# Performance work log

Hardware: AMD Instinct MI355X
Metric: run time of the kernel (lower is better)

## Reference

```python
import jax, jax.numpy as jnp
import numpy as np

B = 4096

def _conv(x, w, s):
    return jax.lax.conv_general_dilated(x, w, (s, s), 'SAME', dimension_numbers=('NHWC', 'HWIO', 'NHWC'))

def _convT(x, w, s):
    return jax.lax.conv_transpose(x, w, (s, s), 'SAME', dimension_numbers=('NHWC', 'HWIO', 'NHWC'))

def _otsu(error):
    # faithful to the TF source: 81 candidate thresholds in [0.1, 0.9],
    # counts of NONZERO masked entries (not simple class counts), NaN-guarded means,
    thresholds = jnp.asarray(np.arange(0.1, 0.91, 0.01), dtype=jnp.float32)  # 81
    hw = error.shape[1] * error.shape[2]
    zero = jnp.zeros(error.shape[0], jnp.float32)

    def step(carry, t):
        sig_max, opti = carry
        below = error < t
        e0 = jnp.where(below, error, 0.0)
        e1 = jnp.where(below, 0.0, error)
        n0 = jnp.sum((e0 != 0).astype(jnp.float32), axis=(1, 2))
        n1 = jnp.sum((e1 != 0).astype(jnp.float32), axis=(1, 2))
        m0 = (jnp.sum(e0, axis=(1, 2)) / hw) * ((n1 + n0) / n0)
        m0 = jnp.where(jnp.isnan(m0), 0.0, m0)
        m1 = (jnp.sum(e1, axis=(1, 2)) / hw) * ((n1 + n0) / n1)
        m1 = jnp.where(jnp.isnan(m1), 0.0, m1)
        p0 = n0 / (n0 + n1)
        p1 = n1 / (n0 + n1)
        sig_b = p0 * p1 * (m0 - m1) ** 2
        upd = sig_b >= sig_max
        return (jnp.where(upd, sig_b, sig_max), jnp.where(upd, t, opti)), None

    (_, opti), _ = jax.lax.scan(step, (zero, zero), thresholds)
    return opti

def _forward(x, eps_noise, ew1, eb1, es1, eo1, ew2, eb2, es2, eo2, ew3, eb3, es3, eo3,
             wzm, bzm, wzl, bzl, dw, db, tw1, tb1, ds1, do1, tw2, tb2, ds2, do2,
             tw3, tb3, ds3, do3, tw4, tb4):
    relu = jax.nn.relu
    # encoder; inference-mode BatchNorm folded into per-channel scale/offset
    h = relu(_conv(x, ew1, 2) + eb1) * es1 + eo1            # [B,16,16,32]
    h = relu(_conv(h, ew2, 2) + eb2) * es2 + eo2            # [B,8,8,64]
    h = relu(_conv(h, ew3, 2) + eb3) * es3 + eo3            # [B,4,4,128]
    h = h.reshape(h.shape[0], -1)                           # [B,2048]
    z_mean = relu(h @ wzm + bzm)
    z_log_var = relu(h @ wzl + bzl)
    z = z_mean + jnp.exp(0.5 * z_log_var) * eps_noise       # Sampling layer
    # decoder (Dropout is identity at inference)
    d = relu(z @ dw + db).reshape(-1, 8, 8, 128)
    d = relu(_convT(d, tw1, 1) + tb1) * ds1 + do1           # [B,8,8,128]
    d = relu(_convT(d, tw2, 2) + tb2) * ds2 + do2           # [B,16,16,64]
    d = relu(_convT(d, tw3, 2) + tb3) * ds3 + do3           # [B,32,32,32]
    recon = jax.nn.sigmoid(_convT(d, tw4, 1) + tb4)         # [B,32,32,3]
    error = jnp.mean((x - recon) ** 2, axis=-1)             # [B,32,32]
    thresh = _otsu(error)                                   # [B]
    return error < thresh[:, None, None]                    # bool mask

def setup_inputs():
    key = jax.random.key(0)
    ks = jax.random.split(key, 12)
    f = jnp.float32
    s = 0.05  # small init scale to keep activations sane
    d = {}
    d['x'] = jax.random.uniform(ks[0], (B, 32, 32, 3), f)
    d['eps_noise'] = jax.random.normal(ks[1], (B, 128), f)
    d['ew1'] = jax.random.normal(ks[2], (5, 5, 3, 32), f) * s
    d['eb1'] = jnp.zeros((32,), f); d['es1'] = jnp.ones((32,), f); d['eo1'] = jnp.zeros((32,), f)
    d['ew2'] = jax.random.normal(ks[3], (5, 5, 32, 64), f) * s
    d['eb2'] = jnp.zeros((64,), f); d['es2'] = jnp.ones((64,), f); d['eo2'] = jnp.zeros((64,), f)
    d['ew3'] = jax.random.normal(ks[4], (5, 5, 64, 128), f) * s
    d['eb3'] = jnp.zeros((128,), f); d['es3'] = jnp.ones((128,), f); d['eo3'] = jnp.zeros((128,), f)
    d['wzm'] = jax.random.normal(ks[5], (2048, 128), f) * s
    d['bzm'] = jnp.zeros((128,), f)
    d['wzl'] = jax.random.normal(ks[6], (2048, 128), f) * s
    d['bzl'] = jnp.zeros((128,), f)
    d['dw'] = jax.random.normal(ks[7], (128, 8192), f) * s
    d['db'] = jnp.zeros((8192,), f)
    d['tw1'] = jax.random.normal(ks[8], (1, 1, 128, 128), f) * s
    d['tb1'] = jnp.zeros((128,), f); d['ds1'] = jnp.ones((128,), f); d['do1'] = jnp.zeros((128,), f)
    d['tw2'] = jax.random.normal(ks[9], (3, 3, 128, 64), f) * s
    d['tb2'] = jnp.zeros((64,), f); d['ds2'] = jnp.ones((64,), f); d['do2'] = jnp.zeros((64,), f)
    d['tw3'] = jax.random.normal(ks[10], (3, 3, 64, 32), f) * s
    d['tb3'] = jnp.zeros((32,), f); d['ds3'] = jnp.ones((32,), f); d['do3'] = jnp.zeros((32,), f)
    d['tw4'] = jax.random.normal(ks[11], (3, 3, 32, 3), f) * s
    d['tb4'] = jnp.zeros((3,), f)
    return d

def reference(x, eps_noise, ew1, eb1, es1, eo1, ew2, eb2, es2, eo2, ew3, eb3, es3, eo3,
              wzm, bzm, wzl, bzl, dw, db, tw1, tb1, ds1, do1, tw2, tb2, ds2, do2,
              tw3, tb3, ds3, do3, tw4, tb4):
    mask = _forward(x, eps_noise, ew1, eb1, es1, eo1, ew2, eb2, es2, eo2, ew3, eb3, es3, eo3,
                    wzm, bzm, wzl, bzl, dw, db, tw1, tb1, ds1, do1, tw2, tb2, ds2, do2,
                    tw3, tb3, ds3, do3, tw4, tb4)
    return mask.astype(jnp.int32)
```

## Files before the change

### kernel.cpp

```cpp
#include <hip/hip_runtime.h>
#include <cstdint>
#include <cstddef>


__global__ __launch_bounds__(256) void k_conv1(const float* __restrict__ x,
    const float* __restrict__ w, const float* __restrict__ bb,
    const float* __restrict__ sc, const float* __restrict__ of,
    float* __restrict__ out) {
  const int b = blockIdx.x;
  const int pos = threadIdx.x;
  const int oy = pos >> 4, ox = pos & 15;
  float acc[32];
#pragma unroll
  for (int c = 0; c < 32; ++c) acc[c] = 0.f;
  const float* xb = x + (size_t)b * 3072;
#pragma unroll 1
  for (int ky = 0; ky < 5; ++ky) {
    const int iy = 2 * oy - 1 + ky;
    if ((unsigned)iy >= 32u) continue;
#pragma unroll 1
    for (int kx = 0; kx < 5; ++kx) {
      const int ix = 2 * ox - 1 + kx;
      if ((unsigned)ix >= 32u) continue;
      const float* xp = xb + (iy * 32 + ix) * 3;
#pragma unroll
      for (int ci = 0; ci < 3; ++ci) {
        const float v = xp[ci];
        const float* wp = w + ((ky * 5 + kx) * 3 + ci) * 32;
#pragma unroll
        for (int c = 0; c < 32; ++c) acc[c] = fmaf(v, wp[c], acc[c]);
      }
    }
  }
  float* op = out + ((size_t)b * 256 + pos) * 32;
#pragma unroll
  for (int c = 0; c < 32; ++c) {
    const float v = fmaxf(acc[c] + bb[c], 0.f);
    op[c] = v * sc[c] + of[c];
  }
}

__global__ __launch_bounds__(256) void k_conv2(const float* __restrict__ in,
    const float* __restrict__ w, const float* __restrict__ bb,
    const float* __restrict__ sc, const float* __restrict__ of,
    float* __restrict__ out) {
  __shared__ float tile[8192];
  const int b = blockIdx.x;
  const int tid = threadIdx.x;
#pragma unroll
  for (int q = 0; q < 8; ++q) {
    const int f4 = tid + q * 256;
    const int pix = f4 >> 3, c4 = (f4 & 7) << 2;
    const float4 v = ((const float4*)(in + (size_t)b * 8192))[f4];
    const int s = ((pix >> 4) * 5 + (pix & 15)) & 31;
    float* dst = &tile[pix * 32];
    dst[(c4 + 0) ^ s] = v.x; dst[(c4 + 1) ^ s] = v.y;
    dst[(c4 + 2) ^ s] = v.z; dst[(c4 + 3) ^ s] = v.w;
  }
  __syncthreads();
  const int pos = tid & 63;
  const int ch = __builtin_amdgcn_readfirstlane(tid >> 6) * 16;
  const int oy = pos >> 3, ox = pos & 7;
  float acc[16];
#pragma unroll
  for (int c = 0; c < 16; ++c) acc[c] = 0.f;
#pragma unroll 1
  for (int ky = 0; ky < 5; ++ky) {
    const int iy = 2 * oy - 1 + ky;
#pragma unroll 1
    for (int kx = 0; kx < 5; ++kx) {
      const int ix = 2 * ox - 1 + kx;
      const bool valid = ((unsigned)iy < 16u) && ((unsigned)ix < 16u);
      const int pix = valid ? (iy * 16 + ix) : 0;
      const int s = ((pix >> 4) * 5 + (pix & 15)) & 31;
      const float* tp = &tile[pix * 32];
      const float* wrow = w + ((ky * 5 + kx) * 32) * 64 + ch;
#pragma unroll 4
      for (int ci = 0; ci < 32; ++ci) {
        float v = tp[ci ^ s];
        v = valid ? v : 0.f;
        const float* wp = wrow + ci * 64;
#pragma unroll
        for (int c = 0; c < 16; ++c) acc[c] = fmaf(v, wp[c], acc[c]);
      }
    }
  }
  float* op = out + ((size_t)b * 64 + pos) * 64 + ch;
#pragma unroll
  for (int c = 0; c < 16; ++c) {
    const float v = fmaxf(acc[c] + bb[ch + c], 0.f);
    op[c] = v * sc[ch + c] + of[ch + c];
  }
}

__global__ __launch_bounds__(512) void k_conv3(const float* __restrict__ in,
    const float* __restrict__ w, const float* __restrict__ bb,
    const float* __restrict__ sc, const float* __restrict__ of,
    float* __restrict__ out) {
  __shared__ float tile[4 * 4096];
  const int b0 = blockIdx.x * 4;
  const int tid = threadIdx.x;
#pragma unroll
  for (int q = 0; q < 8; ++q) {
    const int f4 = tid + q * 512;
    const int img = f4 >> 10, rem = f4 & 1023;
    const int pix = rem >> 4, c4 = (rem & 15) << 2;
    const float4 v = ((const float4*)(in + (size_t)(b0 + img) * 4096))[rem];
    const int s = ((pix >> 3) * 5 + (pix & 7) + img * 9) & 31;
    float* dst = &tile[img * 4096 + pix * 64];
    dst[(c4 + 0) ^ s] = v.x; dst[(c4 + 1) ^ s] = v.y;
    dst[(c4 + 2) ^ s] = v.z; dst[(c4 + 3) ^ s] = v.w;
  }
  __syncthreads();
  const int lane = tid & 63;
  const int pos = lane & 15, img = lane >> 4;
  const int ch = __builtin_amdgcn_readfirstlane(tid >> 6) * 16;
  const int oy = pos >> 2, ox = pos & 3;
  float acc[16];
#pragma unroll
  for (int c = 0; c < 16; ++c) acc[c] = 0.f;
  const float* tb = &tile[img * 4096];
#pragma unroll 1
  for (int ky = 0; ky < 5; ++ky) {
    const int iy = 2 * oy - 1 + ky;
#pragma unroll 1
    for (int kx = 0; kx < 5; ++kx) {
      const int ix = 2 * ox - 1 + kx;
      const bool valid = ((unsigned)iy < 8u) && ((unsigned)ix < 8u);
      const int pix = valid ? (iy * 8 + ix) : 0;
      const int s = ((pix >> 3) * 5 + (pix & 7) + img * 9) & 31;
      const float* tp = tb + pix * 64;
      const float* wrow = w + ((ky * 5 + kx) * 64) * 128 + ch;
#pragma unroll 4
      for (int ci = 0; ci < 64; ++ci) {
        float v = tp[ci ^ s];
        v = valid ? v : 0.f;
        const float* wp = wrow + ci * 128;
#pragma unroll
        for (int c = 0; c < 16; ++c) acc[c] = fmaf(v, wp[c], acc[c]);
      }
    }
  }
  float* op = out + ((size_t)(b0 + img) * 16 + pos) * 128 + ch;
#pragma unroll
  for (int c = 0; c < 16; ++c) {
    const float v = fmaxf(acc[c] + bb[ch + c], 0.f);
    op[c] = v * sc[ch + c] + of[ch + c];
  }
}

__global__ __launch_bounds__(256) void k_fcz(const float* __restrict__ h3,
    const float* __restrict__ wzm, const float* __restrict__ bzm,
    const float* __restrict__ wzl, const float* __restrict__ bzl,
    const float* __restrict__ eps, float* __restrict__ z) {
  __shared__ float a[4 * 256];
  const int ib = blockIdx.x * 4;
  const int tid = threadIdx.x;
  const int co = tid & 127;
  const int grp = __builtin_amdgcn_readfirstlane(tid >> 7);
  float am[2], al[2];
#pragma unroll
  for (int i = 0; i < 2; ++i) { am[i] = 0.f; al[i] = 0.f; }
  for (int kc = 0; kc < 2048; kc += 256) {
    __syncthreads();
    {
      const int r = tid >> 6, c4 = (tid & 63) << 2;
      *(float4*)&a[r * 256 + c4] =
          *(const float4*)&h3[(size_t)(ib + r) * 2048 + kc + c4];
    }
    __syncthreads();
#pragma unroll 4
    for (int k = 0; k < 256; k += 4) {
      float wm[4], wl[4];
#pragma unroll
      for (int q = 0; q < 4; ++q) {
        wm[q] = wzm[(size_t)(kc + k + q) * 128 + co];
        wl[q] = wzl[(size_t)(kc + k + q) * 128 + co];
      }
#pragma unroll
      for (int i = 0; i < 2; ++i) {
        const float4 av = *(const float4*)&a[(grp * 2 + i) * 256 + k];
        am[i] = fmaf(av.x, wm[0], am[i]); am[i] = fmaf(av.y, wm[1], am[i]);
        am[i] = fmaf(av.z, wm[2], am[i]); am[i] = fmaf(av.w, wm[3], am[i]);
        al[i] = fmaf(av.x, wl[0], al[i]); al[i] = fmaf(av.y, wl[1], al[i]);
        al[i] = fmaf(av.z, wl[2], al[i]); al[i] = fmaf(av.w, wl[3], al[i]);
      }
    }
  }
#pragma unroll
  for (int i = 0; i < 2; ++i) {
    const int row = ib + grp * 2 + i;
    const float zm = fmaxf(am[i] + bzm[co], 0.f);
    const float zl = fmaxf(al[i] + bzl[co], 0.f);
    z[(size_t)row * 128 + co] = zm + expf(0.5f * zl) * eps[(size_t)row * 128 + co];
  }
}

__global__ __launch_bounds__(256) void k_fcdec(const float* __restrict__ z,
    const float* __restrict__ dw, const float* __restrict__ db,
    float* __restrict__ out) {
  __shared__ float zt[64 * 128];
  const int bid = blockIdx.x;
  const int m0 = (bid >> 6) * 64;
  const int n0 = (bid & 63) * 128;
  const int tid = threadIdx.x;
#pragma unroll
  for (int q = 0; q < 8; ++q) {
    const int f4 = tid + q * 256;
    const int img = f4 >> 5, c4 = (f4 & 31) << 2;
    const float4 v = *(const float4*)&z[(size_t)(m0 + img) * 128 + c4];
    const int s = img & 31;
    float* dst = &zt[img * 128];
    dst[(c4 + 0) ^ s] = v.x; dst[(c4 + 1) ^ s] = v.y;
    dst[(c4 + 2) ^ s] = v.z; dst[(c4 + 3) ^ s] = v.w;
  }
  __syncthreads();
  const int img = tid & 63;
  const int grp = __builtin_amdgcn_readfirstlane(tid >> 6);
  const int nb = n0 + grp * 32;
  float acc[32];
#pragma unroll
  for (int c = 0; c < 32; ++c) acc[c] = 0.f;
  const float* zrow = &zt[img * 128];
  const int s = img & 31;
#pragma unroll 4
  for (int k = 0; k < 128; ++k) {
    const float v = zrow[k ^ s];
    const float* wp = dw + (size_t)k * 8192 + nb;
#pragma unroll
    for (int c = 0; c < 32; ++c) acc[c] = fmaf(v, wp[c], acc[c]);
  }
  float* op = out + (size_t)(m0 + img) * 8192 + nb;
#pragma unroll
  for (int c = 0; c < 32; ++c) op[c] = fmaxf(acc[c] + db[nb + c], 0.f);
}

__global__ __launch_bounds__(256) void k_tconv1(const float* __restrict__ in,
    const float* __restrict__ w, const float* __restrict__ bb,
    const float* __restrict__ sc, const float* __restrict__ of,
    float* __restrict__ out) {
  __shared__ float tile[8192];
  const int b = blockIdx.x;
  const int tid = threadIdx.x;
#pragma unroll
  for (int q = 0; q < 8; ++q) {
    const int f4 = tid + q * 256;
    const int pix = f4 >> 5, c4 = (f4 & 31) << 2;
    const float4 v = ((const float4*)(in + (size_t)b * 8192))[f4];
    const int s = pix & 31;
    float* dst = &tile[pix * 128];
    dst[(c4 + 0) ^ s] = v.x; dst[(c4 + 1) ^ s] = v.y;
    dst[(c4 + 2) ^ s] = v.z; dst[(c4 + 3) ^ s] = v.w;
  }
  __syncthreads();
  const int pos = tid & 63;
  const int ch = __builtin_amdgcn_readfirstlane((tid >> 6) * 32);
  const float* trow = &tile[pos * 128];
  const int s = pos & 31;
  float acc[32];
#pragma unroll
  for (int c = 0; c < 32; ++c) acc[c] = 0.f;
#pragma unroll 4
  for (int ci = 0; ci < 128; ++ci) {
    const float v = trow[ci ^ s];
    const float* wp = w + ci * 128 + ch;
#pragma unroll
    for (int c = 0; c < 32; ++c) acc[c] = fmaf(v, wp[c], acc[c]);
  }
  float* op = out + ((size_t)b * 64 + pos) * 128 + ch;
#pragma unroll
  for (int c = 0; c < 32; ++c) {
    const float v = fmaxf(acc[c] + bb[ch + c], 0.f);
    op[c] = v * sc[ch + c] + of[ch + c];
  }
}

__global__ __launch_bounds__(256) void k_tconv2(const float* __restrict__ in,
    const float* __restrict__ w, const float* __restrict__ bb,
    const float* __restrict__ sc, const float* __restrict__ of,
    float* __restrict__ out) {
  __shared__ float tile[64 * 128];
  const int b = blockIdx.x;
  const int tid = threadIdx.x;
#pragma unroll
  for (int q = 0; q < 8; ++q) {
    const int f4 = tid + q * 256;
    const int pix = f4 >> 5, c4 = (f4 & 31) << 2;
    const float4 v = ((const float4*)(in + (size_t)b * 8192))[f4];
    const int s = ((pix >> 3) * 5 + (pix & 7)) & 31;
    float* dst = &tile[pix * 128];
    dst[(c4 + 0) ^ s] = v.x; dst[(c4 + 1) ^ s] = v.y;
    dst[(c4 + 2) ^ s] = v.z; dst[(c4 + 3) ^ s] = v.w;
  }
  __syncthreads();
  const int lane = tid & 63;
  const int ch = __builtin_amdgcn_readfirstlane((tid >> 6) * 16);
  const int jy = lane >> 3, jx = lane & 7;
  float acc[4][16];
#pragma unroll
  for (int p = 0; p < 4; ++p)
#pragma unroll
    for (int c = 0; c < 16; ++c) acc[p][c] = 0.f;
  const int DY[9]  = {1,1,0,0,1,0,0,0,0};
  const int DX[9]  = {1,0,1,0,0,0,1,0,0};
  const int KYt[9] = {0,0,2,2,0,2,1,1,1};
  const int KXt[9] = {0,2,0,2,1,1,0,2,1};
  const int PHt[9] = {0,0,0,0,1,1,2,2,3};
#pragma unroll
  for (int t = 0; t < 9; ++t) {
    const int sy = jy - DY[t], sx = jx - DX[t];
    const bool valid = (sy >= 0) && (sx >= 0);
    const int pix = valid ? (sy * 8 + sx) : 0;
    const int s = ((pix >> 3) * 5 + (pix & 7)) & 31;
    const float* tp = &tile[pix * 128];
    const float* wrow = w + ((KYt[t] * 3 + KXt[t]) * 128) * 64 + ch;
#pragma unroll 4
    for (int ci = 0; ci < 128; ++ci) {
      float v = tp[ci ^ s];
      v = valid ? v : 0.f;
      const float* wp = wrow + ci * 64;
#pragma unroll
      for (int c = 0; c < 16; ++c)
        acc[PHt[t]][c] = fmaf(v, wp[c], acc[PHt[t]][c]);
    }
  }
#pragma unroll
  for (int py = 0; py < 2; ++py)
#pragma unroll
    for (int px = 0; px < 2; ++px) {
      const int oy = 2 * jy + py, ox = 2 * jx + px;
      float* op = out + (((size_t)b * 16 + oy) * 16 + ox) * 64 + ch;
#pragma unroll
      for (int c = 0; c < 16; ++c) {
        const float v = fmaxf(acc[py * 2 + px][c] + bb[ch + c], 0.f);
        op[c] = v * sc[ch + c] + of[ch + c];
      }
    }
}

__global__ __launch_bounds__(256) void k_tconv3(const float* __restrict__ in,
    const float* __restrict__ w, const float* __restrict__ bb,
    const float* __restrict__ sc, const float* __restrict__ of,
    float* __restrict__ out) {
  __shared__ float tile[9 * 16 * 64];
  const int b = blockIdx.x >> 1;
  const int r0 = (blockIdx.x & 1) * 8;
  const int tid = threadIdx.x;
#pragma unroll
  for (int q = 0; q < 9; ++q) {
    const int f4 = tid + q * 256;
    const int rr = f4 >> 8, rem = f4 & 255;
    const int col = rem >> 4, c4 = (rem & 15) << 2;
    const int gy = r0 - 1 + rr;
    float4 v = make_float4(0.f, 0.f, 0.f, 0.f);
    if (gy >= 0)
      v = *(const float4*)&in[(((size_t)b * 16 + gy) * 16 + col) * 64 + c4];
    const int s = (rr * 5 + col) & 31;
    float* dst = &tile[(rr * 16 + col) * 64];
    dst[(c4 + 0) ^ s] = v.x; dst[(c4 + 1) ^ s] = v.y;
    dst[(c4 + 2) ^ s] = v.z; dst[(c4 + 3) ^ s] = v.w;
  }
  __syncthreads();
  const int pos = tid & 127;
  const int jy = pos >> 4, jx = pos & 15;
  const int ch = __builtin_amdgcn_readfirstlane(tid >> 7) * 16;
  float acc[4][16];
#pragma unroll
  for (int p = 0; p < 4; ++p)
#pragma unroll
    for (int c = 0; c < 16; ++c) acc[p][c] = 0.f;
  const int DY[9]  = {1,1,0,0,1,0,0,0,0};
  const int DX[9]  = {1,0,1,0,0,0,1,0,0};
  const int KYt[9] = {0,0,2,2,0,2,1,1,1};
  const int KXt[9] = {0,2,0,2,1,1,0,2,1};
  const int PHt[9] = {0,0,0,0,1,1,2,2,3};
#pragma unroll
  for (int t = 0; t < 9; ++t) {
    const int syst = jy + 1 - DY[t];
    const int sx = jx - DX[t];
    const bool valid = (sx >= 0);
    const int sxc = valid ? sx : 0;
    const int s = (syst * 5 + sxc) & 31;
    const float* tp = &tile[(syst * 16 + sxc) * 64];
    const float* wrow = w + ((KYt[t] * 3 + KXt[t]) * 64) * 32 + ch;
#pragma unroll 2
    for (int ci = 0; ci < 64; ++ci) {
      float v = tp[ci ^ s];
      v = valid ? v : 0.f;
      const float* wp = wrow + ci * 32;
#pragma unroll
      for (int c = 0; c < 16; ++c)
        acc[PHt[t]][c] = fmaf(v, wp[c], acc[PHt[t]][c]);
    }
  }
  const int gy = r0 + jy;
#pragma unroll
  for (int py = 0; py < 2; ++py)
#pragma unroll
    for (int px = 0; px < 2; ++px) {
      const int oy = 2 * gy + py, ox = 2 * jx + px;
      float* op = out + (((size_t)b * 32 + oy) * 32 + ox) * 32 + ch;
#pragma unroll
      for (int c = 0; c < 16; ++c) {
        const float v = fmaxf(acc[py * 2 + px][c] + bb[ch + c], 0.f);
        op[c] = v * sc[ch + c] + of[ch + c];
      }
    }
}

__global__ __launch_bounds__(128) void k_tconv4err(const float* __restrict__ t3,
    const float* __restrict__ w, const float* __restrict__ bb,
    const float* __restrict__ x, float* __restrict__ err) {
  __shared__ float tile[32 * 340];
  const int b = blockIdx.x >> 2;
  const int r0 = (blockIdx.x & 3) * 8;
  const int tid = threadIdx.x;
  for (int f4 = tid; f4 < 2560; f4 += 128) {
    const int rr = f4 >> 8, rem = f4 & 255;
    const int px = rem >> 3, c4 = (rem & 7) << 2;
    const int gy = r0 - 1 + rr;
    float4 v = make_float4(0.f, 0.f, 0.f, 0.f);
    if ((unsigned)gy < 32u)
      v = *(const float4*)&t3[(((size_t)b * 32 + gy) * 32 + px) * 32 + c4];
    tile[(c4 + 0) * 340 + rr * 34 + px] = v.x;
    tile[(c4 + 1) * 340 + rr * 34 + px] = v.y;
    tile[(c4 + 2) * 340 + rr * 34 + px] = v.z;
    tile[(c4 + 3) * 340 + rr * 34 + px] = v.w;
  }
  __syncthreads();
  const int tx = tid & 31, ty = tid >> 5;
  float acc[2][3];
#pragma unroll
  for (int d = 0; d < 2; ++d)
#pragma unroll
    for (int c = 0; c < 3; ++c) acc[d][c] = 0.f;
#pragma unroll 2
  for (int ci = 0; ci < 32; ++ci) {
    float p[4][3];
#pragma unroll
    for (int r = 0; r < 4; ++r)
#pragma unroll
      for (int cx = 0; cx < 3; ++cx) {
        const int lx = tx + cx - 1;
        float v = 0.f;
        if ((unsigned)lx < 32u) v = tile[ci * 340 + (ty * 2 + r) * 34 + lx];
        p[r][cx] = v;
      }
#pragma unroll
    for (int ky = 0; ky < 3; ++ky)
#pragma unroll
      for (int kx = 0; kx < 3; ++kx) {
        const float* wp = w + ((ky * 3 + kx) * 32 + ci) * 3;
#pragma unroll
        for (int dy = 0; dy < 2; ++dy) {
          const float v = p[dy + ky][kx];
          acc[dy][0] = fmaf(v, wp[0], acc[dy][0]);
          acc[dy][1] = fmaf(v, wp[1], acc[dy][1]);
          acc[dy][2] = fmaf(v, wp[2], acc[dy][2]);
        }
      }
  }
#pragma unroll
  for (int dy = 0; dy < 2; ++dy) {
    const int oy = r0 + ty * 2 + dy;
    const size_t pidx = (size_t)b * 1024 + oy * 32 + tx;
    float e = 0.f;
#pragma unroll
    for (int c = 0; c < 3; ++c) {
      const float pre = acc[dy][c] + bb[c];
      float r;
      if (pre >= 0.f) {
        r = 1.f / (1.f + expf(-pre));
      } else {
        const float ex = expf(pre);
        r = ex / (1.f + ex);
      }
      const float dd = x[pidx * 3 + c] - r;
      e += dd * dd;
    }
    err[pidx] = e / 3.0f;
  }
}

__global__ __launch_bounds__(256) void k_otsu(const float* __restrict__ err,
                                              int* __restrict__ outmask) {
  __shared__ float e[2][1024];
  __shared__ float sig[2][81];
  __shared__ float opti[2];
  const int b0 = blockIdx.x * 2;
  const int tid = threadIdx.x;
  for (int f4 = tid; f4 < 512; f4 += 256) {
    const int img = f4 >> 8, idx = (f4 & 255) << 2;
    *(float4*)&e[img][idx] = *(const float4*)&err[(size_t)(b0 + img) * 1024 + idx];
  }
  __syncthreads();
  const int img = tid >> 7, j = tid & 127;
  if (j < 81) {
    const float t = (float)(0.1 + (double)j * 0.01);
    float n0 = 0.f, n1 = 0.f, s0 = 0.f, s1 = 0.f;
    for (int i = 0; i < 1024; ++i) {
      const float v = e[img][i];
      if (v < t) {
        if (v != 0.f) { n0 += 1.f; s0 += v; }
      } else {
        n1 += 1.f; s1 += v;
      }
    }
    const float nt = n0 + n1;
    float m0 = (s0 / 1024.f) * (nt / n0);
    if (m0 != m0) m0 = 0.f;
    float m1 = (s1 / 1024.f) * (nt / n1);
    if (m1 != m1) m1 = 0.f;
    const float p0 = n0 / nt, p1 = n1 / nt;
    const float dm = m0 - m1;
    sig[img][j] = p0 * p1 * (dm * dm);
  }
  __syncthreads();
  if (j == 0) {
    float smax = 0.f, op = 0.f;
    for (int jj = 0; jj < 81; ++jj) {
      const float sb = sig[img][jj];
      const float t = (float)(0.1 + (double)jj * 0.01);
      if (sb >= smax) { smax = sb; op = t; }
    }
    opti[img] = op;
  }
  __syncthreads();
#pragma unroll
  for (int q = 0; q < 8; ++q) {
    const int idx = tid + q * 256;
    const int im = idx >> 10, p = idx & 1023;
    outmask[(size_t)(b0 + im) * 1024 + p] = (e[im][p] < opti[im]) ? 1 : 0;
  }
}

extern "C" void kernel_launch(void* const* d_in, const int* in_sizes, int n_in,
                              void* d_out, int out_size, void* d_ws, size_t ws_size,
                              hipStream_t stream) {
  (void)in_sizes; (void)n_in; (void)out_size;
  const float* x    = (const float*)d_in[0];
  const float* eps  = (const float*)d_in[1];
  const float* ew1  = (const float*)d_in[2];
  const float* eb1  = (const float*)d_in[3];
  const float* es1  = (const float*)d_in[4];
  const float* eo1  = (const float*)d_in[5];
  const float* ew2  = (const float*)d_in[6];
  const float* eb2  = (const float*)d_in[7];
  const float* es2  = (const float*)d_in[8];
  const float* eo2  = (const float*)d_in[9];
  const float* ew3  = (const float*)d_in[10];
  const float* eb3  = (const float*)d_in[11];
  const float* es3  = (const float*)d_in[12];
  const float* eo3  = (const float*)d_in[13];
  const float* wzm  = (const float*)d_in[14];
  const float* bzm  = (const float*)d_in[15];
  const float* wzl  = (const float*)d_in[16];
  const float* bzl  = (const float*)d_in[17];
  const float* dw   = (const float*)d_in[18];
  const float* db   = (const float*)d_in[19];
  const float* tw1  = (const float*)d_in[20];
  const float* tb1  = (const float*)d_in[21];
  const float* ds1  = (const float*)d_in[22];
  const float* do1  = (const float*)d_in[23];
  const float* tw2  = (const float*)d_in[24];
  const float* tb2  = (const float*)d_in[25];
  const float* ds2  = (const float*)d_in[26];
  const float* do2  = (const float*)d_in[27];
  const float* tw3  = (const float*)d_in[28];
  const float* tb3  = (const float*)d_in[29];
  const float* ds3  = (const float*)d_in[30];
  const float* do3  = (const float*)d_in[31];
  const float* tw4  = (const float*)d_in[32];
  const float* tb4  = (const float*)d_in[33];
  int* mask = (int*)d_out;

  const size_t per_img_bytes = 233472;
  int C = 64;
  const int cand[6] = {4096, 2048, 1024, 512, 256, 128};
  for (int i = 0; i < 6; ++i) {
    if ((size_t)cand[i] * per_img_bytes <= ws_size) { C = cand[i]; break; }
  }

  float* p0 = (float*)d_ws;
  float* p1 = p0 + (size_t)C * 32768;
  float* p2 = p1 + (size_t)C * 8192;
  float* p3 = p2 + (size_t)C * 16384;

  for (int c0 = 0; c0 < 4096; c0 += C) {
    const float* xc   = x   + (size_t)c0 * 3072;
    const float* epsc = eps + (size_t)c0 * 128;
    int*         mc   = mask + (size_t)c0 * 1024;
    float* h1 = p0;  float* dd = p0;  float* t3 = p0;
    float* h2 = p1;  float* zz = p1;  float* t1 = p1;
    float* h3 = p2;  float* t2 = p2;
    float* er = p3;

    k_conv1    <<<C,      256, 0, stream>>>(xc, ew1, eb1, es1, eo1, h1);
    k_conv2    <<<C,      256, 0, stream>>>(h1, ew2, eb2, es2, eo2, h2);
    k_conv3    <<<C / 4,  512, 0, stream>>>(h2, ew3, eb3, es3, eo3, h3);
    k_fcz      <<<C / 4,  256, 0, stream>>>(h3, wzm, bzm, wzl, bzl, epsc, zz);
    k_fcdec    <<<C,      256, 0, stream>>>(zz, dw, db, dd);
    k_tconv1   <<<C,      256, 0, stream>>>(dd, tw1, tb1, ds1, do1, t1);
    k_tconv2   <<<C,      256, 0, stream>>>(t1, tw2, tb2, ds2, do2, t2);
    k_tconv3   <<<C * 2,  256, 0, stream>>>(t2, tw3, tb3, ds3, do3, t3);
    k_tconv4err<<<C * 4,  128, 0, stream>>>(t3, tw4, tb4, xc, er);
    k_otsu     <<<C / 2,  256, 0, stream>>>(er, mc);
  }
}
```

Measured before the change: 4.349 ms.

## Vectorize LDS reads as float4 and restructure decoder tail convolutions

Result: slower. 5.088 ms (+17.0%).

```diff
diff --git a/kernel.cpp b/kernel.cpp
--- a/kernel.cpp
+++ b/kernel.cpp
@@ -44,22 +44,20 @@
     const float* __restrict__ w, const float* __restrict__ bb,
     const float* __restrict__ sc, const float* __restrict__ of,
     float* __restrict__ out) {
-  __shared__ float tile[8192];
+  __shared__ float4 tile4[2048];
   const int b = blockIdx.x;
   const int tid = threadIdx.x;
 #pragma unroll
   for (int q = 0; q < 8; ++q) {
     const int f4 = tid + q * 256;
-    const int pix = f4 >> 3, c4 = (f4 & 7) << 2;
-    const float4 v = ((const float4*)(in + (size_t)b * 8192))[f4];
-    const int s = ((pix >> 4) * 5 + (pix & 15)) & 31;
-    float* dst = &tile[pix * 32];
-    dst[(c4 + 0) ^ s] = v.x; dst[(c4 + 1) ^ s] = v.y;
-    dst[(c4 + 2) ^ s] = v.z; dst[(c4 + 3) ^ s] = v.w;
+    const int pix = f4 >> 3, g4 = f4 & 7;
+    const int s4 = (((pix >> 4) * 5) + (pix & 15)) & 7;
+    tile4[pix * 8 + (g4 ^ s4)] = ((const float4*)(in + (size_t)b * 8192))[f4];
   }
   __syncthreads();
   const int pos = tid & 63;
-  const int ch = __builtin_amdgcn_readfirstlane(tid >> 6) * 16;
+  const int chg = __builtin_amdgcn_readfirstlane(tid >> 6);
+  const int co0 = chg * 16;
   const int oy = pos >> 3, ox = pos & 7;
   float acc[16];
 #pragma unroll
@@ -72,24 +70,28 @@
       const int ix = 2 * ox - 1 + kx;
       const bool valid = ((unsigned)iy < 16u) && ((unsigned)ix < 16u);
       const int pix = valid ? (iy * 16 + ix) : 0;
-      const int s = ((pix >> 4) * 5 + (pix & 15)) & 31;
-      const float* tp = &tile[pix * 32];
-      const float* wrow = w + ((ky * 5 + kx) * 32) * 64 + ch;
-#pragma unroll 4
-      for (int ci = 0; ci < 32; ++ci) {
-        float v = tp[ci ^ s];
-        v = valid ? v : 0.f;
-        const float* wp = wrow + ci * 64;
-#pragma unroll
-        for (int c = 0; c < 16; ++c) acc[c] = fmaf(v, wp[c], acc[c]);
-      }
-    }
-  }
-  float* op = out + ((size_t)b * 64 + pos) * 64 + ch;
+      const int s4 = (((pix >> 4) * 5) + (pix & 15)) & 7;
+      const float* wt = w + ((size_t)(ky * 5 + kx) * 32) * 64 + co0;
+#pragma unroll
+      for (int g4 = 0; g4 < 8; ++g4) {
+        float4 a = tile4[pix * 8 + (g4 ^ s4)];
+        a.x = valid ? a.x : 0.f; a.y = valid ? a.y : 0.f;
+        a.z = valid ? a.z : 0.f; a.w = valid ? a.w : 0.f;
+        const float av[4] = {a.x, a.y, a.z, a.w};
+#pragma unroll
+        for (int j = 0; j < 4; ++j) {
+          const float* wp = wt + (g4 * 4 + j) * 64;
+#pragma unroll
+          for (int c = 0; c < 16; ++c) acc[c] = fmaf(av[j], wp[c], acc[c]);
+        }
+      }
+    }
+  }
+  float* op = out + ((size_t)b * 64 + pos) * 64 + co0;
 #pragma unroll
   for (int c = 0; c < 16; ++c) {
-    const float v = fmaxf(acc[c] + bb[ch + c], 0.f);
-    op[c] = v * sc[ch + c] + of[ch + c];
+    const float v = fmaxf(acc[c] + bb[co0 + c], 0.f);
+    op[c] = v * sc[co0 + c] + of[co0 + c];
   }
 }
 
@@ -97,29 +99,28 @@
     const float* __restrict__ w, const float* __restrict__ bb,
     const float* __restrict__ sc, const float* __restrict__ of,
     float* __restrict__ out) {
-  __shared__ float tile[4 * 4096];
+  __shared__ float4 tile4[4096];
   const int b0 = blockIdx.x * 4;
   const int tid = threadIdx.x;
 #pragma unroll
   for (int q = 0; q < 8; ++q) {
     const int f4 = tid + q * 512;
     const int img = f4 >> 10, rem = f4 & 1023;
-    const int pix = rem >> 4, c4 = (rem & 15) << 2;
-    const float4 v = ((const float4*)(in + (size_t)(b0 + img) * 4096))[rem];
-    const int s = ((pix >> 3) * 5 + (pix & 7) + img * 9) & 31;
-    float* dst = &tile[img * 4096 + pix * 64];
-    dst[(c4 + 0) ^ s] = v.x; dst[(c4 + 1) ^ s] = v.y;
-    dst[(c4 + 2) ^ s] = v.z; dst[(c4 + 3) ^ s] = v.w;
+    const int pix = rem >> 4, g4 = rem & 15;
+    const int s4 = (((pix >> 3) * 5) + (pix & 7) + img * 3) & 15;
+    tile4[img * 1024 + pix * 16 + (g4 ^ s4)] =
+        ((const float4*)(in + (size_t)(b0 + img) * 4096))[rem];
   }
   __syncthreads();
   const int lane = tid & 63;
-  const int pos = lane & 15, img = lane >> 4;
-  const int ch = __builtin_amdgcn_readfirstlane(tid >> 6) * 16;
+  const int img = lane >> 4, pos = lane & 15;
+  const int chg = __builtin_amdgcn_readfirstlane(tid >> 6);
+  const int co0 = chg * 16;
   const int oy = pos >> 2, ox = pos & 3;
   float acc[16];
 #pragma unroll
   for (int c = 0; c < 16; ++c) acc[c] = 0.f;
-  const float* tb = &tile[img * 4096];
+  const float4* tb = &tile4[img * 1024];
 #pragma unroll 1
   for (int ky = 0; ky < 5; ++ky) {
     const int iy = 2 * oy - 1 + ky;
@@ -128,24 +129,28 @@
       const int ix = 2 * ox - 1 + kx;
       const bool valid = ((unsigned)iy < 8u) && ((unsigned)ix < 8u);
       const int pix = valid ? (iy * 8 + ix) : 0;
-      const int s = ((pix >> 3) * 5 + (pix & 7) + img * 9) & 31;
-      const float* tp = tb + pix * 64;
-      const float* wrow = w + ((ky * 5 + kx) * 64) * 128 + ch;
-#pragma unroll 4
-      for (int ci = 0; ci < 64; ++ci) {
-        float v = tp[ci ^ s];
-        v = valid ? v : 0.f;
-        const float* wp = wrow + ci * 128;
-#pragma unroll
-        for (int c = 0; c < 16; ++c) acc[c] = fmaf(v, wp[c], acc[c]);
-      }
-    }
-  }
-  float* op = out + ((size_t)(b0 + img) * 16 + pos) * 128 + ch;
+      const int s4 = (((pix >> 3) * 5) + (pix & 7) + img * 3) & 15;
+      const float* wt = w + ((size_t)(ky * 5 + kx) * 64) * 128 + co0;
+#pragma unroll
+      for (int g4 = 0; g4 < 16; ++g4) {
+        float4 a = tb[pix * 16 + (g4 ^ s4)];
+        a.x = valid ? a.x : 0.f; a.y = valid ? a.y : 0.f;
+        a.z = valid ? a.z : 0.f; a.w = valid ? a.w : 0.f;
+        const float av[4] = {a.x, a.y, a.z, a.w};
+#pragma unroll
+        for (int j = 0; j < 4; ++j) {
+          const float* wp = wt + (g4 * 4 + j) * 128;
+#pragma unroll
+          for (int c = 0; c < 16; ++c) acc[c] = fmaf(av[j], wp[c], acc[c]);
+        }
+      }
+    }
+  }
+  float* op = out + ((size_t)(b0 + img) * 16 + pos) * 128 + co0;
 #pragma unroll
   for (int c = 0; c < 16; ++c) {
-    const float v = fmaxf(acc[c] + bb[ch + c], 0.f);
-    op[c] = v * sc[ch + c] + of[ch + c];
+    const float v = fmaxf(acc[c] + bb[co0 + c], 0.f);
+    op[c] = v * sc[co0 + c] + of[co0 + c];
   }
 }
 
@@ -199,7 +204,7 @@
 __global__ __launch_bounds__(256) void k_fcdec(const float* __restrict__ z,
     const float* __restrict__ dw, const float* __restrict__ db,
     float* __restrict__ out) {
-  __shared__ float zt[64 * 128];
+  __shared__ float4 zt4[2048];
   const int bid = blockIdx.x;
   const int m0 = (bid >> 6) * 64;
   const int n0 = (bid & 63) * 128;
@@ -207,28 +212,28 @@
 #pragma unroll
   for (int q = 0; q < 8; ++q) {
     const int f4 = tid + q * 256;
-    const int img = f4 >> 5, c4 = (f4 & 31) << 2;
-    const float4 v = *(const float4*)&z[(size_t)(m0 + img) * 128 + c4];
-    const int s = img & 31;
-    float* dst = &zt[img * 128];
-    dst[(c4 + 0) ^ s] = v.x; dst[(c4 + 1) ^ s] = v.y;
-    dst[(c4 + 2) ^ s] = v.z; dst[(c4 + 3) ^ s] = v.w;
+    const int img = f4 >> 5, g4 = f4 & 31;
+    const int s4 = (img * 5) & 31;
+    zt4[img * 32 + (g4 ^ s4)] = ((const float4*)(z + (size_t)(m0) * 128))[f4];
   }
   __syncthreads();
   const int img = tid & 63;
   const int grp = __builtin_amdgcn_readfirstlane(tid >> 6);
   const int nb = n0 + grp * 32;
+  const int s4 = (img * 5) & 31;
   float acc[32];
 #pragma unroll
   for (int c = 0; c < 32; ++c) acc[c] = 0.f;
-  const float* zrow = &zt[img * 128];
-  const int s = img & 31;
-#pragma unroll 4
-  for (int k = 0; k < 128; ++k) {
-    const float v = zrow[k ^ s];
-    const float* wp = dw + (size_t)k * 8192 + nb;
-#pragma unroll
-    for (int c = 0; c < 32; ++c) acc[c] = fmaf(v, wp[c], acc[c]);
+#pragma unroll
+  for (int g4 = 0; g4 < 32; ++g4) {
+    const float4 a = zt4[img * 32 + (g4 ^ s4)];
+    const float av[4] = {a.x, a.y, a.z, a.w};
+#pragma unroll
+    for (int j = 0; j < 4; ++j) {
+      const float* wp = dw + (size_t)(g4 * 4 + j) * 8192 + nb;
+#pragma unroll
+      for (int c = 0; c < 32; ++c) acc[c] = fmaf(av[j], wp[c], acc[c]);
+    }
   }
   float* op = out + (size_t)(m0 + img) * 8192 + nb;
 #pragma unroll
@@ -239,39 +244,40 @@
     const float* __restrict__ w, const float* __restrict__ bb,
     const float* __restrict__ sc, const float* __restrict__ of,
     float* __restrict__ out) {
-  __shared__ float tile[8192];
+  __shared__ float4 tile4[2048];
   const int b = blockIdx.x;
   const int tid = threadIdx.x;
 #pragma unroll
   for (int q = 0; q < 8; ++q) {
     const int f4 = tid + q * 256;
-    const int pix = f4 >> 5, c4 = (f4 & 31) << 2;
-    const float4 v = ((const float4*)(in + (size_t)b * 8192))[f4];
-    const int s = pix & 31;
-    float* dst = &tile[pix * 128];
-    dst[(c4 + 0) ^ s] = v.x; dst[(c4 + 1) ^ s] = v.y;
-    dst[(c4 + 2) ^ s] = v.z; dst[(c4 + 3) ^ s] = v.w;
+    const int pix = f4 >> 5, g4 = f4 & 31;
+    const int s4 = (pix * 5) & 31;
+    tile4[pix * 32 + (g4 ^ s4)] = ((const float4*)(in + (size_t)b * 8192))[f4];
   }
   __syncthreads();
   const int pos = tid & 63;
-  const int ch = __builtin_amdgcn_readfirstlane((tid >> 6) * 32);
-  const float* trow = &tile[pos * 128];
-  const int s = pos & 31;
+  const int chg = __builtin_amdgcn_readfirstlane(tid >> 6);
+  const int co0 = chg * 32;
+  const int s4 = (pos * 5) & 31;
   float acc[32];
 #pragma unroll
   for (int c = 0; c < 32; ++c) acc[c] = 0.f;
-#pragma unroll 4
-  for (int ci = 0; ci < 128; ++ci) {
-    const float v = trow[ci ^ s];
-    const float* wp = w + ci * 128 + ch;
-#pragma unroll
-    for (int c = 0; c < 32; ++c) acc[c] = fmaf(v, wp[c], acc[c]);
-  }
-  float* op = out + ((size_t)b * 64 + pos) * 128 + ch;
+#pragma unroll
+  for (int g4 = 0; g4 < 32; ++g4) {
+    const float4 a = tile4[pos * 32 + (g4 ^ s4)];
+    const float av[4] = {a.x, a.y, a.z, a.w};
+#pragma unroll
+    for (int j = 0; j < 4; ++j) {
+      const float* wp = w + (g4 * 4 + j) * 128 + co0;
+#pragma unroll
+      for (int c = 0; c < 32; ++c) acc[c] = fmaf(av[j], wp[c], acc[c]);
+    }
+  }
+  float* op = out + ((size_t)b * 64 + pos) * 128 + co0;
 #pragma unroll
   for (int c = 0; c < 32; ++c) {
-    const float v = fmaxf(acc[c] + bb[ch + c], 0.f);
-    op[c] = v * sc[ch + c] + of[ch + c];
+    const float v = fmaxf(acc[c] + bb[co0 + c], 0.f);
+    op[c] = v * sc[co0 + c] + of[co0 + c];
   }
 }
 
@@ -279,23 +285,21 @@
     const float* __restrict__ w, const float* __restrict__ bb,
     const float* __restrict__ sc, const float* __restrict__ of,
     float* __restrict__ out) {
-  __shared__ float tile[64 * 128];
+  __shared__ float4 tile4[2048];
   const int b = blockIdx.x;
   const int tid = threadIdx.x;
 #pragma unroll
   for (int q = 0; q < 8; ++q) {
     const int f4 = tid + q * 256;
-    const int pix = f4 >> 5, c4 = (f4 & 31) << 2;
-    const float4 v = ((const float4*)(in + (size_t)b * 8192))[f4];
-    const int s = ((pix >> 3) * 5 + (pix & 7)) & 31;
-    float* dst = &tile[pix * 128];
-    dst[(c4 + 0) ^ s] = v.x; dst[(c4 + 1) ^ s] = v.y;
-    dst[(c4 + 2) ^ s] = v.z; dst[(c4 + 3) ^ s] = v.w;
-  }
-  __syncthreads();
-  const int lane = tid & 63;
-  const int ch = __builtin_amdgcn_readfirstlane((tid >> 6) * 16);
-  const int jy = lane >> 3, jx = lane & 7;
+    const int pix = f4 >> 5, g4 = f4 & 31;
+    const int s4 = (pix * 5) & 31;
+    tile4[pix * 32 + (g4 ^ s4)] = ((const float4*)(in + (size_t)b * 8192))[f4];
+  }
+  __syncthreads();
+  const int pos = tid & 63;
+  const int chg = __builtin_amdgcn_readfirstlane(tid >> 6);
+  const int co0 = chg * 16;
+  const int jy = pos >> 3, jx = pos & 7;
   float acc[4][16];
 #pragma unroll
   for (int p = 0; p < 4; ++p)
@@ -306,22 +310,26 @@
   const int KYt[9] = {0,0,2,2,0,2,1,1,1};
   const int KXt[9] = {0,2,0,2,1,1,0,2,1};
   const int PHt[9] = {0,0,0,0,1,1,2,2,3};
-#pragma unroll
+#pragma unroll 1
   for (int t = 0; t < 9; ++t) {
     const int sy = jy - DY[t], sx = jx - DX[t];
     const bool valid = (sy >= 0) && (sx >= 0);
     const int pix = valid ? (sy * 8 + sx) : 0;
-    const int s = ((pix >> 3) * 5 + (pix & 7)) & 31;
-    const float* tp = &tile[pix * 128];
-    const float* wrow = w + ((KYt[t] * 3 + KXt[t]) * 128) * 64 + ch;
-#pragma unroll 4
-    for (int ci = 0; ci < 128; ++ci) {
-      float v = tp[ci ^ s];
-      v = valid ? v : 0.f;
-      const float* wp = wrow + ci * 64;
-#pragma unroll
-      for (int c = 0; c < 16; ++c)
-        acc[PHt[t]][c] = fmaf(v, wp[c], acc[PHt[t]][c]);
+    const int s4 = (pix * 5) & 31;
+    const int ph = PHt[t];
+    const float* wt = w + ((size_t)(KYt[t] * 3 + KXt[t]) * 128) * 64 + co0;
+#pragma unroll
+    for (int g4 = 0; g4 < 32; ++g4) {
+      float4 a = tile4[pix * 32 + (g4 ^ s4)];
+      a.x = valid ? a.x : 0.f; a.y = valid ? a.y : 0.f;
+      a.z = valid ? a.z : 0.f; a.w = valid ? a.w : 0.f;
+      const float av[4] = {a.x, a.y, a.z, a.w};
+#pragma unroll
+      for (int j = 0; j < 4; ++j) {
+        const float* wp = wt + (g4 * 4 + j) * 64;
+#pragma unroll
+        for (int c = 0; c < 16; ++c) acc[ph][c] = fmaf(av[j], wp[c], acc[ph][c]);
+      }
     }
   }
 #pragma unroll
@@ -329,157 +337,179 @@
 #pragma unroll
     for (int px = 0; px < 2; ++px) {
       const int oy = 2 * jy + py, ox = 2 * jx + px;
-      float* op = out + (((size_t)b * 16 + oy) * 16 + ox) * 64 + ch;
+      float* op = out + (((size_t)b * 16 + oy) * 16 + ox) * 64 + co0;
 #pragma unroll
       for (int c = 0; c < 16; ++c) {
-        const float v = fmaxf(acc[py * 2 + px][c] + bb[ch + c], 0.f);
-        op[c] = v * sc[ch + c] + of[ch + c];
-      }
-    }
-}
-
-__global__ __launch_bounds__(256) void k_tconv3(const float* __restrict__ in,
+        const float v = fmaxf(acc[py * 2 + px][c] + bb[co0 + c], 0.f);
+        op[c] = v * sc[co0 + c] + of[co0 + c];
+      }
+    }
+}
+
+__global__ __launch_bounds__(512) void k_tconv3(const float* __restrict__ in,
     const float* __restrict__ w, const float* __restrict__ bb,
     const float* __restrict__ sc, const float* __restrict__ of,
-    float* __restrict__ out) {
-  __shared__ float tile[9 * 16 * 64];
+    float* __restrict__ t3g) {
+  __shared__ float4 tile4[145 * 16];
   const int b = blockIdx.x >> 1;
   const int r0 = (blockIdx.x & 1) * 8;
   const int tid = threadIdx.x;
-#pragma unroll
-  for (int q = 0; q < 9; ++q) {
-    const int f4 = tid + q * 256;
-    const int rr = f4 >> 8, rem = f4 & 255;
-    const int col = rem >> 4, c4 = (rem & 15) << 2;
+  for (int f4 = tid; f4 < 2304; f4 += 512) {
+    const int rr = f4 >> 8;
+    const int col = (f4 >> 4) & 15, g4 = f4 & 15;
     const int gy = r0 - 1 + rr;
     float4 v = make_float4(0.f, 0.f, 0.f, 0.f);
     if (gy >= 0)
-      v = *(const float4*)&in[(((size_t)b * 16 + gy) * 16 + col) * 64 + c4];
-    const int s = (rr * 5 + col) & 31;
-    float* dst = &tile[(rr * 16 + col) * 64];
-    dst[(c4 + 0) ^ s] = v.x; dst[(c4 + 1) ^ s] = v.y;
-    dst[(c4 + 2) ^ s] = v.z; dst[(c4 + 3) ^ s] = v.w;
-  }
+      v = *(const float4*)&in[(((size_t)b * 16 + gy) * 16 + col) * 64 + g4 * 4];
+    const int s4 = (rr * 5 + col) & 15;
+    tile4[(rr * 16 + col) * 16 + (g4 ^ s4)] = v;
+  }
+  if (tid < 16) tile4[144 * 16 + tid] = make_float4(0.f, 0.f, 0.f, 0.f);
   __syncthreads();
   const int pos = tid & 127;
-  const int jy = pos >> 4, jx = pos & 15;
-  const int ch = __builtin_amdgcn_readfirstlane(tid >> 7) * 16;
-  float acc[4][16];
+  const int prow = pos >> 4, pcol = pos & 15;
+  const int chg = __builtin_amdgcn_readfirstlane(tid >> 7);
+  const int co0 = chg * 8;
+  float acc[4][8];
 #pragma unroll
   for (int p = 0; p < 4; ++p)
 #pragma unroll
-    for (int c = 0; c < 16; ++c) acc[p][c] = 0.f;
+    for (int c = 0; c < 8; ++c) acc[p][c] = 0.f;
   const int DY[9]  = {1,1,0,0,1,0,0,0,0};
   const int DX[9]  = {1,0,1,0,0,0,1,0,0};
   const int KYt[9] = {0,0,2,2,0,2,1,1,1};
   const int KXt[9] = {0,2,0,2,1,1,0,2,1};
   const int PHt[9] = {0,0,0,0,1,1,2,2,3};
-#pragma unroll
+#pragma unroll 1
   for (int t = 0; t < 9; ++t) {
-    const int syst = jy + 1 - DY[t];
-    const int sx = jx - DX[t];
-    const bool valid = (sx >= 0);
-    const int sxc = valid ? sx : 0;
-    const int s = (syst * 5 + sxc) & 31;
-    const float* tp = &tile[(syst * 16 + sxc) * 64];
-    const float* wrow = w + ((KYt[t] * 3 + KXt[t]) * 64) * 32 + ch;
-#pragma unroll 2
-    for (int ci = 0; ci < 64; ++ci) {
-      float v = tp[ci ^ s];
-      v = valid ? v : 0.f;
-      const float* wp = wrow + ci * 32;
-#pragma unroll
-      for (int c = 0; c < 16; ++c)
-        acc[PHt[t]][c] = fmaf(v, wp[c], acc[PHt[t]][c]);
-    }
-  }
-  const int gy = r0 + jy;
+    const int syst = prow + 1 - DY[t];
+    const int sx = pcol - DX[t];
+    const bool vx = (sx >= 0);
+    const int pix = vx ? (syst * 16 + sx) : 144;
+    const int s4 = vx ? ((syst * 5 + sx) & 15) : 0;
+    const int ph = PHt[t];
+    const float* wt = w + ((size_t)(KYt[t] * 3 + KXt[t]) * 64) * 32 + co0;
+#pragma unroll
+    for (int g4 = 0; g4 < 16; ++g4) {
+      const float4 a = tile4[pix * 16 + (g4 ^ s4)];
+      const float av[4] = {a.x, a.y, a.z, a.w};
+#pragma unroll
+      for (int j = 0; j < 4; ++j) {
+        const float* wp = wt + (g4 * 4 + j) * 32;
+#pragma unroll
+        for (int c = 0; c < 8; ++c) acc[ph][c] = fmaf(av[j], wp[c], acc[ph][c]);
+      }
+    }
+  }
+  const int jy = r0 + prow;
 #pragma unroll
   for (int py = 0; py < 2; ++py)
 #pragma unroll
     for (int px = 0; px < 2; ++px) {
-      const int oy = 2 * gy + py, ox = 2 * jx + px;
-      float* op = out + (((size_t)b * 32 + oy) * 32 + ox) * 32 + ch;
-#pragma unroll
-      for (int c = 0; c < 16; ++c) {
-        const float v = fmaxf(acc[py * 2 + px][c] + bb[ch + c], 0.f);
-        op[c] = v * sc[ch + c] + of[ch + c];
-      }
-    }
-}
-
-__global__ __launch_bounds__(128) void k_tconv4err(const float* __restrict__ t3,
+      const int oy = 2 * jy + py, ox = 2 * pcol + px;
+      float* op = t3g + ((size_t)b * 4 + chg) * 8192 + (size_t)(oy * 32 + ox) * 8;
+      float vv[8];
+#pragma unroll
+      for (int c = 0; c < 8; ++c) {
+        const float v = fmaxf(acc[py * 2 + px][c] + bb[co0 + c], 0.f);
+        vv[c] = v * sc[co0 + c] + of[co0 + c];
+      }
+      *(float4*)&op[0] = make_float4(vv[0], vv[1], vv[2], vv[3]);
+      *(float4*)&op[4] = make_float4(vv[4], vv[5], vv[6], vv[7]);
+    }
+}
+
+__global__ __launch_bounds__(256) void k_tconv4err(const float* __restrict__ t3g,
     const float* __restrict__ w, const float* __restrict__ bb,
     const float* __restrict__ x, float* __restrict__ err) {
-  __shared__ float tile[32 * 340];
-  const int b = blockIdx.x >> 2;
-  const int r0 = (blockIdx.x & 3) * 8;
-  const int tid = threadIdx.x;
-  for (int f4 = tid; f4 < 2560; f4 += 128) {
-    const int rr = f4 >> 8, rem = f4 & 255;
-    const int px = rem >> 3, c4 = (rem & 7) << 2;
-    const int gy = r0 - 1 + rr;
-    float4 v = make_float4(0.f, 0.f, 0.f, 0.f);
-    if ((unsigned)gy < 32u)
-      v = *(const float4*)&t3[(((size_t)b * 32 + gy) * 32 + px) * 32 + c4];
-    tile[(c4 + 0) * 340 + rr * 34 + px] = v.x;
-    tile[(c4 + 1) * 340 + rr * 34 + px] = v.y;
-    tile[(c4 + 2) * 340 + rr * 34 + px] = v.z;
-    tile[(c4 + 3) * 340 + rr * 34 + px] = v.w;
-  }
-  __syncthreads();
-  const int tx = tid & 31, ty = tid >> 5;
-  float acc[2][3];
-#pragma unroll
-  for (int d = 0; d < 2; ++d)
-#pragma unroll
-    for (int c = 0; c < 3; ++c) acc[d][c] = 0.f;
-#pragma unroll 2
-  for (int ci = 0; ci < 32; ++ci) {
-    float p[4][3];
-#pragma unroll
-    for (int r = 0; r < 4; ++r)
-#pragma unroll
-      for (int cx = 0; cx < 3; ++cx) {
-        const int lx = tx + cx - 1;
-        float v = 0.f;
-        if ((unsigned)lx < 32u) v = tile[ci * 340 + (ty * 2 + r) * 34 + lx];
-        p[r][cx] = v;
-      }
-#pragma unroll
-    for (int ky = 0; ky < 3; ++ky)
-#pragma unroll
-      for (int kx = 0; kx < 3; ++kx) {
-        const float* wp = w + ((ky * 3 + kx) * 32 + ci) * 3;
-#pragma unroll
-        for (int dy = 0; dy < 2; ++dy) {
-          const float v = p[dy + ky][kx];
-          acc[dy][0] = fmaf(v, wp[0], acc[dy][0]);
-          acc[dy][1] = fmaf(v, wp[1], acc[dy][1]);
-          acc[dy][2] = fmaf(v, wp[2], acc[dy][2]);
+  __shared__ float4 win4[34 * 65];
+  const int b = blockIdx.x;
+  const int tid = threadIdx.x;
+  const int ty = tid >> 4, tx = tid & 15;
+  float acc[2][2][3];
+#pragma unroll
+  for (int dy = 0; dy < 2; ++dy)
+#pragma unroll
+    for (int dx = 0; dx < 2; ++dx)
+#pragma unroll
+      for (int c = 0; c < 3; ++c) acc[dy][dx][c] = 0.f;
+#pragma unroll 1
+  for (int g = 0; g < 4; ++g) {
+    __syncthreads();
+    for (int f4 = tid; f4 < 2176; f4 += 256) {
+      const int rr = f4 >> 6;
+      const int rem = f4 & 63;
+      const int col = rem >> 1, h = rem & 1;
+      const int gy = rr - 1;
+      float4 v = make_float4(0.f, 0.f, 0.f, 0.f);
+      if ((unsigned)gy < 32u)
+        v = ((const float4*)(t3g + ((size_t)b * 4 + g) * 8192))[(gy * 32 + col) * 2 + h];
+      win4[rr * 65 + col * 2 + h] = v;
+    }
+    __syncthreads();
+#pragma unroll 1
+    for (int h = 0; h < 2; ++h) {
+      float4 W[4][4];
+#pragma unroll
+      for (int wy = 0; wy < 4; ++wy)
+#pragma unroll
+        for (int wx = 0; wx < 4; ++wx) {
+          const int col = 2 * tx - 1 + wx;
+          const bool edge = (wx == 0) || (wx == 3);
+          const bool v = edge ? ((unsigned)col < 32u) : true;
+          const int cc = v ? col : 0;
+          float4 t = win4[(2 * ty + wy) * 65 + cc * 2 + h];
+          if (edge) {
+            t.x = v ? t.x : 0.f; t.y = v ? t.y : 0.f;
+            t.z = v ? t.z : 0.f; t.w = v ? t.w : 0.f;
+          }
+          W[wy][wx] = t;
         }
-      }
-  }
-#pragma unroll
-  for (int dy = 0; dy < 2; ++dy) {
-    const int oy = r0 + ty * 2 + dy;
-    const size_t pidx = (size_t)b * 1024 + oy * 32 + tx;
-    float e = 0.f;
-#pragma unroll
-    for (int c = 0; c < 3; ++c) {
-      const float pre = acc[dy][c] + bb[c];
-      float r;
-      if (pre >= 0.f) {
-        r = 1.f / (1.f + expf(-pre));
-      } else {
-        const float ex = expf(pre);
-        r = ex / (1.f + ex);
-      }
-      const float dd = x[pidx * 3 + c] - r;
-      e += dd * dd;
-    }
-    err[pidx] = e / 3.0f;
-  }
+#pragma unroll
+      for (int j = 0; j < 4; ++j) {
+        const int ci = g * 8 + h * 4 + j;
+#pragma unroll
+        for (int ky = 0; ky < 3; ++ky)
+#pragma unroll
+          for (int kx = 0; kx < 3; ++kx) {
+            const float* wp = w + ((ky * 3 + kx) * 32 + ci) * 3;
+            const float w0 = wp[0], w1 = wp[1], w2 = wp[2];
+#pragma unroll
+            for (int dy = 0; dy < 2; ++dy)
+#pragma unroll
+              for (int dx = 0; dx < 2; ++dx) {
+                const float4 t = W[dy + ky][dx + kx];
+                const float av = (j == 0) ? t.x : (j == 1) ? t.y : (j == 2) ? t.z : t.w;
+                acc[dy][dx][0] = fmaf(av, w0, acc[dy][dx][0]);
+                acc[dy][dx][1] = fmaf(av, w1, acc[dy][dx][1]);
+                acc[dy][dx][2] = fmaf(av, w2, acc[dy][dx][2]);
+              }
+          }
+      }
+    }
+  }
+#pragma unroll
+  for (int dy = 0; dy < 2; ++dy)
+#pragma unroll
+    for (int dx = 0; dx < 2; ++dx) {
+      const int oy = 2 * ty + dy, ox = 2 * tx + dx;
+      const size_t pidx = (size_t)b * 1024 + oy * 32 + ox;
+      float e = 0.f;
+#pragma unroll
+      for (int c = 0; c < 3; ++c) {
+        const float pre = acc[dy][dx][c] + bb[c];
+        float r;
+        if (pre >= 0.f) {
+          r = 1.f / (1.f + expf(-pre));
+        } else {
+          const float ex = expf(pre);
+          r = ex / (1.f + ex);
+        }
+        const float dd = x[pidx * 3 + c] - r;
+        e += dd * dd;
+      }
+      err[pidx] = e / 3.0f;
+    }
 }
 
 __global__ __launch_bounds__(256) void k_otsu(const float* __restrict__ err,
@@ -602,8 +632,8 @@
     k_fcdec    <<<C,      256, 0, stream>>>(zz, dw, db, dd);
     k_tconv1   <<<C,      256, 0, stream>>>(dd, tw1, tb1, ds1, do1, t1);
     k_tconv2   <<<C,      256, 0, stream>>>(t1, tw2, tb2, ds2, do2, t2);
-    k_tconv3   <<<C * 2,  256, 0, stream>>>(t2, tw3, tb3, ds3, do3, t3);
-    k_tconv4err<<<C * 4,  128, 0, stream>>>(t3, tw4, tb4, xc, er);
+    k_tconv3   <<<C * 2,  512, 0, stream>>>(t2, tw3, tb3, ds3, do3, t3);
+    k_tconv4err<<<C,      256, 0, stream>>>(t3, tw4, tb4, xc, er);
     k_otsu     <<<C / 2,  256, 0, stream>>>(er, mc);
   }
 }
```
